# Kernel optimization log

Hardware: AMD Instinct MI355X
Metric: run time of the kernel (lower is better)

## Reference

```python
import jax, jax.numpy as jnp
import numpy as np

B = 32                 # decode batch (sequences)
NBLK = 128             # blocks per sequence
BLOCK = 16             # tokens per block
H, D = 16, 128         # heads, head_dim
HID = H * D            # 2048
FFN = 8192
VOCAB = 32000
MAXPOS = 8192
KV_LEN = NBLK * BLOCK  # 2048 max context
NUM_BLOCKS = B * NBLK  # 4096
ROPE_THETA = 10000.0


def _rope_cos_sin(pos):
    # pos: [...] int -> cos, sin: [..., D//2]
    inv_freq = 1.0 / (ROPE_THETA ** (jnp.arange(0, D, 2, dtype=jnp.float32) / D))
    ang = pos.astype(jnp.float32)[..., None] * inv_freq
    return jnp.cos(ang), jnp.sin(ang)


def _apply_rope(x, cos, sin):
    # x: [..., D]; cos/sin broadcastable to [..., D//2]; half-split (Llama) rotation
    x1, x2 = jnp.split(x, 2, axis=-1)
    return jnp.concatenate([x1 * cos - x2 * sin, x1 * sin + x2 * cos], axis=-1)


def setup_inputs() -> dict:
    key = jax.random.key(0)
    ks = jax.random.split(key, 12)
    inp = {
        "input_ids": jax.random.randint(ks[0], (B,), 0, VOCAB),
        "positions": jax.random.randint(ks[1], (B,), 0, KV_LEN),
        "kv_cache": jax.random.normal(ks[2], (NUM_BLOCKS, 2, BLOCK, H, D), jnp.float32),
        "block_tables": jnp.arange(NUM_BLOCKS, dtype=jnp.int32).reshape(B, NBLK),
        "context_lens": jax.random.randint(ks[3], (B,), 1, KV_LEN + 1).astype(jnp.int32),
        "embed_tokens": jax.random.normal(ks[4], (VOCAB, HID), jnp.float32) * 0.02,
        "embed_positions": jax.random.normal(ks[5], (MAXPOS, HID), jnp.float32) * 0.02,
        "Wq": jax.random.normal(ks[6], (HID, HID), jnp.float32) / np.float32(np.sqrt(HID)),
        "Wo": jax.random.normal(ks[7], (HID, HID), jnp.float32) / np.float32(np.sqrt(HID)),
        "Wprm": jax.random.normal(ks[8], (HID, HID), jnp.float32) / np.float32(np.sqrt(HID)),
        "W1": jax.random.normal(ks[9], (HID, FFN), jnp.float32) / np.float32(np.sqrt(HID)),
        "W2": jax.random.normal(ks[10], (FFN, HID), jnp.float32) / np.float32(np.sqrt(FFN)),
    }
    return inp


def reference(input_ids, positions, kv_cache, block_tables, context_lens,
              embed_tokens, embed_positions, Wq, Wo, Wprm, W1, W2):
    # token + position embeddings -> [B, HID]
    emb = embed_tokens[input_ids] + embed_positions[positions]

    # query projection with RoPE at the current position (fused RoPE on q)
    q = (emb @ Wq).reshape(B, H, D)
    cos_q, sin_q = _rope_cos_sin(positions)            # [B, D/2]
    q = _apply_rope(q, cos_q[:, None, :], sin_q[:, None, :])

    # paged KV gather: [B, NBLK, 2, BLOCK, H, D]
    kv = kv_cache[block_tables]
    k = kv[:, :, 0].reshape(B, KV_LEN, H, D)
    v = kv[:, :, 1].reshape(B, KV_LEN, H, D)

    # inline RoPE on gathered keys at their cache positions
    tok_pos = jnp.arange(KV_LEN)
    cos_k, sin_k = _rope_cos_sin(tok_pos)              # [S, D/2]
    k = _apply_rope(k, cos_k[None, :, None, :], sin_k[None, :, None, :])

    # decode attention over valid context
    scale = jnp.asarray(D, jnp.float32) ** -0.5
    scores = jnp.einsum("bhd,bshd->bhs", q, k) * scale
    valid = tok_pos[None, :] < context_lens[:, None]   # [B, S]
    scores = jnp.where(valid[:, None, :], scores, jnp.float32(-1e30))
    probs = jax.nn.softmax(scores, axis=-1)
    attn = jnp.einsum("bhs,bshd->bhd", probs, v).reshape(B, HID) @ Wo

    # PRM head + FFN (no activation in source), residual combine
    prm_scores = attn @ Wprm
    ffn_output = (attn @ W1) @ W2
    return ffn_output + prm_scores
```

## Files before the change

kernel.cpp:

```cpp
#include <hip/hip_runtime.h>
#include <hip/hip_bf16.h>
#include <math.h>

#define BATCH   32
#define NBLK    128
#define BLOCK_T 16
#define HEADS   16
#define DHEAD   128
#define HID     2048
#define FFN     8192
#define KV_LEN  2048

#define NSPLIT2 64
#define TOKSPL  32

__global__ void prep_kernel(const int* __restrict__ ids, const int* __restrict__ pos,
                            const float* __restrict__ et, const float* __restrict__ ep,
                            float* __restrict__ c4f, float* __restrict__ s4f,
                            float* __restrict__ emb) {
    if (blockIdx.x < 512) {
        int s = blockIdx.x * 4 + (threadIdx.x >> 6);
        int i = threadIdx.x & 63;
        float inv = powf(10000.0f, -(float)i / 64.0f);
        float ang = (float)s * inv;
        c4f[s * 64 + i] = cosf(ang);
        s4f[s * 64 + i] = sinf(ang);
    } else {
        int b = blockIdx.x - 512;
        int id = ids[b], p = pos[b];
        const float4* a = (const float4*)(et + (size_t)id * HID);
        const float4* d = (const float4*)(ep + (size_t)p * HID);
        float4* o = (float4*)(emb + (size_t)b * HID);
        for (int c = threadIdx.x; c < HID / 4; c += 256) {
            float4 x = a[c], y = d[c];
            o[c] = make_float4(x.x + y.x, x.y + y.y, x.z + y.z, x.w + y.w);
        }
    }
}

template <int KC>
__device__ __forceinline__ void gemm2_body(
    const float* __restrict__ X, const float* __restrict__ W,
    float* __restrict__ P, int K, int N, int bx, int by, int tid) {
    __shared__ float xs[KC][36];
    const int k0 = by * KC;
    const int j  = bx * 512 + tid * 2;

    #pragma unroll
    for (int t = tid; t < 32 * KC / 4; t += 256) {
        int bb = t / (KC / 4), qq = t % (KC / 4);
        float4 xv = *reinterpret_cast<const float4*>(X + (size_t)bb * K + k0 + 4 * qq);
        xs[4 * qq + 0][bb] = xv.x; xs[4 * qq + 1][bb] = xv.y;
        xs[4 * qq + 2][bb] = xv.z; xs[4 * qq + 3][bb] = xv.w;
    }
    __syncthreads();

    float acc[32][2];
    #pragma unroll
    for (int bb = 0; bb < 32; ++bb) { acc[bb][0] = 0.f; acc[bb][1] = 0.f; }

    const float* wp = W + (size_t)k0 * N + j;
    float2 bufA[16], bufB[16];
    #pragma unroll
    for (int u = 0; u < 16; ++u)
        bufA[u] = *reinterpret_cast<const float2*>(wp + (size_t)u * N);

    #define G2_FMA16(BUF, KK)                                                   \
        _Pragma("unroll")                                                       \
        for (int u = 0; u < 16; ++u) {                                          \
            const float2 w = BUF[u];                                            \
            _Pragma("unroll")                                                   \
            for (int g = 0; g < 8; ++g) {                                       \
                const float4 xv = *reinterpret_cast<const float4*>(&xs[(KK) + u][g * 4]); \
                acc[4*g+0][0] = fmaf(xv.x, w.x, acc[4*g+0][0]);                 \
                acc[4*g+0][1] = fmaf(xv.x, w.y, acc[4*g+0][1]);                 \
                acc[4*g+1][0] = fmaf(xv.y, w.x, acc[4*g+1][0]);                 \
                acc[4*g+1][1] = fmaf(xv.y, w.y, acc[4*g+1][1]);                 \
                acc[4*g+2][0] = fmaf(xv.z, w.x, acc[4*g+2][0]);                 \
                acc[4*g+2][1] = fmaf(xv.z, w.y, acc[4*g+2][1]);                 \
                acc[4*g+3][0] = fmaf(xv.w, w.x, acc[4*g+3][0]);                 \
                acc[4*g+3][1] = fmaf(xv.w, w.y, acc[4*g+3][1]);                 \
            }                                                                   \
        }

    for (int kk = 0; kk < KC; kk += 32) {
        #pragma unroll
        for (int u = 0; u < 16; ++u)
            bufB[u] = *reinterpret_cast<const float2*>(wp + (size_t)(kk + 16 + u) * N);
        G2_FMA16(bufA, kk)
        #pragma unroll
        for (int u = 0; u < 16; ++u) {
            int rr = kk + 32 + u; rr = (rr < KC) ? rr : (KC - 1);
            bufA[u] = *reinterpret_cast<const float2*>(wp + (size_t)rr * N);
        }
        G2_FMA16(bufB, kk + 16)
    }
    #undef G2_FMA16

    float* pp = P + ((size_t)by * 32) * N + j;
    #pragma unroll
    for (int bb = 0; bb < 32; ++bb)
        *reinterpret_cast<float2*>(pp + (size_t)bb * N) = make_float2(acc[bb][0], acc[bb][1]);
}

template <int KC>
__global__ __launch_bounds__(256) void gemm2_kernel(
    const float* __restrict__ X, const float* __restrict__ W,
    float* __restrict__ P, int K, int N) {
    gemm2_body<KC>(X, W, P, K, N, blockIdx.x, blockIdx.y, threadIdx.x);
}

__global__ __launch_bounds__(256) void gemm2_dual_kernel(
    const float* __restrict__ X, const float* __restrict__ Wprm,
    const float* __restrict__ W1,
    float* __restrict__ Pprm, float* __restrict__ P1) {
    if (blockIdx.x < 256) {
        gemm2_body<32>(X, Wprm, Pprm, HID, HID, blockIdx.x & 3, blockIdx.x >> 2, threadIdx.x);
    } else {
        int bb = blockIdx.x - 256;
        gemm2_body<128>(X, W1, P1, HID, FFN, bb & 15, bb >> 4, threadIdx.x);
    }
}

__global__ void red_stage1(const float* __restrict__ PA, const float* __restrict__ PB,
                           int ngA, float* __restrict__ S, int total4) {
    int idx4 = blockIdx.x * 256 + threadIdx.x;
    if (idx4 >= total4) return;
    int g = blockIdx.y;
    const float4* src = (const float4*)((g < ngA) ? PA : PB);
    int c0 = ((g < ngA) ? g : (g - ngA)) * 8;
    float4 s = make_float4(0.f, 0.f, 0.f, 0.f);
    #pragma unroll
    for (int c = 0; c < 8; ++c) {
        float4 v = src[(size_t)(c0 + c) * total4 + idx4];
        s.x += v.x; s.y += v.y; s.z += v.z; s.w += v.w;
    }
    ((float4*)S)[(size_t)g * total4 + idx4] = s;
}

__global__ void red_stage2(const float* __restrict__ S, int ng, int total4,
                           float* __restrict__ out) {
    int idx4 = blockIdx.x * 256 + threadIdx.x;
    if (idx4 >= total4) return;
    float4 s = make_float4(0.f, 0.f, 0.f, 0.f);
    for (int g = 0; g < ng; ++g) {
        float4 v = ((const float4*)S)[(size_t)g * total4 + idx4];
        s.x += v.x; s.y += v.y; s.z += v.z; s.w += v.w;
    }
    ((float4*)out)[idx4] = s;
}

__global__ void reduce4_kernel(const float* __restrict__ P, int nch, int total4,
                               float* __restrict__ out) {
    int idx4 = blockIdx.x * 256 + threadIdx.x;
    if (idx4 >= total4) return;
    const float4* P4 = (const float4*)P;
    float4 s = make_float4(0.f, 0.f, 0.f, 0.f);
    for (int c = 0; c < nch; ++c) {
        float4 v = P4[(size_t)c * total4 + idx4];
        s.x += v.x; s.y += v.y; s.z += v.z; s.w += v.w;
    }
    ((float4*)out)[idx4] = s;
}

__global__ void rope_q_from_S(const float* __restrict__ S, int ng,
                              const int* __restrict__ positions,
                              const float* __restrict__ c4f, const float* __restrict__ s4f,
                              float* __restrict__ qout) {
    int idx = blockIdx.x * 256 + threadIdx.x;
    int i = idx & 63, hh = (idx >> 6) & 15, b = idx >> 10;
    int base = b * HID + hh * DHEAD;
    float q1 = 0.f, q2 = 0.f;
    for (int g = 0; g < ng; ++g) {
        q1 += S[(size_t)g * (BATCH * HID) + base + i];
        q2 += S[(size_t)g * (BATCH * HID) + base + 64 + i];
    }
    int pos = positions[b];
    float co = c4f[pos * 64 + i], si = s4f[pos * 64 + i];
    qout[base + i]      = q1 * co - q2 * si;
    qout[base + 64 + i] = q1 * si + q2 * co;
}

__global__ __launch_bounds__(512) void attn_partial_kernel(
    const float* __restrict__ q, const float* __restrict__ kv,
    const int* __restrict__ block_tables, const int* __restrict__ context_lens,
    const float* __restrict__ c4f, const float* __restrict__ s4f,
    float* __restrict__ pm, float* __restrict__ pl, float* __restrict__ pacc) {
    const int idx = blockIdx.x;
    const int split = idx & (NSPLIT2 - 1);
    const int b = idx >> 6;
    const int tid = threadIdx.x;
    const int h = tid >> 5;
    const int l5 = tid & 31;

    const int ctx = context_lens[b];
    const int s_begin = split * TOKSPL;
    const int len = min(TOKSPL, ctx - s_begin);

    const int bt0 = block_tables[b * NBLK + split * 2];
    const int bt1 = block_tables[b * NBLK + split * 2 + 1];

    const int out_idx = (b * HEADS + h) * NSPLIT2 + split;

    const float4 qr = *reinterpret_cast<const float4*>(q + b * HID + h * DHEAD + 4 * l5);
    const float sgn2 = (l5 & 16) ? -1.f : 1.f;
    const int fq4 = (l5 & 15) * 4;
    float4 pqs;
    pqs.x = sgn2 * __shfl_xor(qr.x, 16); pqs.y = sgn2 * __shfl_xor(qr.y, 16);
    pqs.z = sgn2 * __shfl_xor(qr.z, 16); pqs.w = sgn2 * __shfl_xor(qr.w, 16);

    float m = -INFINITY, l = 0.f;
    float4 a4 = make_float4(0.f, 0.f, 0.f, 0.f);

    if (len > 0) {
        const int NI = (len + 3) & ~3;

        #define LOADT(T, K4, V4, C4, S4) {                                         \
            int tc = min((T), len - 1);                                            \
            int blk = (tc & 16) ? bt1 : bt0;                                       \
            const float* kp = kv + (size_t)blk * 65536                             \
                                 + (size_t)(tc & 15) * 2048 + h * DHEAD;           \
            K4 = *reinterpret_cast<const float4*>(kp + 4 * l5);                    \
            V4 = *reinterpret_cast<const float4*>(kp + 32768 + 4 * l5);            \
            C4 = *reinterpret_cast<const float4*>(c4f + (size_t)(s_begin + tc) * 64 + fq4); \
            S4 = *reinterpret_cast<const float4*>(s4f + (size_t)(s_begin + tc) * 64 + fq4); \
        }

        #define PROCT(T, K4, V4, C4, S4) {                                         \
            float cfx = fmaf(pqs.x, S4.x, qr.x * C4.x);                            \
            float cfy = fmaf(pqs.y, S4.y, qr.y * C4.y);                            \
            float cfz = fmaf(pqs.z, S4.z, qr.z * C4.z);                            \
            float cfw = fmaf(pqs.w, S4.w, qr.w * C4.w);                            \
            float dot = fmaf(K4.x, cfx, fmaf(K4.y, cfy, fmaf(K4.z, cfz, K4.w * cfw))); \
            dot += __shfl_xor(dot, 1);  dot += __shfl_xor(dot, 2);                 \
            dot += __shfl_xor(dot, 4);  dot += __shfl_xor(dot, 8);                 \
            dot += __shfl_xor(dot, 16);                                            \
            float d = ((T) < len) ? dot * 0.08838834764831845f : -INFINITY;        \
            float mn = fmaxf(m, d);                                                \
            float ms = fmaxf(mn, -3.0e38f);                                        \
            float corr = __expf(m - ms);                                           \
            float e = __expf(d - ms);                                              \
            l = l * corr + e;                                                      \
            a4.x = fmaf(e, V4.x, a4.x * corr);                                     \
            a4.y = fmaf(e, V4.y, a4.y * corr);                                     \
            a4.z = fmaf(e, V4.z, a4.z * corr);                                     \
            a4.w = fmaf(e, V4.w, a4.w * corr);                                     \
            m = mn;                                                                \
        }

        float4 kA, vA, cA, sA, kB, vB, cB, sB;
        float4 kC, vC, cC, sC, kD, vD, cD, sD;
        LOADT(0, kA, vA, cA, sA);
        LOADT(1, kB, vB, cB, sB);
        LOADT(2, kC, vC, cC, sC);
        LOADT(3, kD, vD, cD, sD);

        for (int t = 0; t < NI; t += 4) {
            PROCT(t,     kA, vA, cA, sA);  LOADT(t + 4, kA, vA, cA, sA);
            PROCT(t + 1, kB, vB, cB, sB);  LOADT(t + 5, kB, vB, cB, sB);
            PROCT(t + 2, kC, vC, cC, sC);  LOADT(t + 6, kC, vC, cC, sC);
            PROCT(t + 3, kD, vD, cD, sD);  LOADT(t + 7, kD, vD, cD, sD);
        }
        #undef LOADT
        #undef PROCT
    }

    if (l5 == 0) { pm[out_idx] = m; pl[out_idx] = l; }
    *reinterpret_cast<float4*>(pacc + (size_t)out_idx * 128 + 4 * l5) = a4;
}

__global__ void attn_combine_kernel(const float* __restrict__ pm, const float* __restrict__ pl,
                                    const float* __restrict__ pacc, float* __restrict__ attn_out) {
    const int bh = blockIdx.x;
    const int l5 = threadIdx.x;
    if (l5 >= 32) return;
    const int base = bh * NSPLIT2;
    float M = -INFINITY;
    for (int sp = 0; sp < NSPLIT2; ++sp) M = fmaxf(M, pm[base + sp]);
    float L = 0.f;
    float4 o = make_float4(0.f, 0.f, 0.f, 0.f);
    for (int sp = 0; sp < NSPLIT2; ++sp) {
        float mv = pm[base + sp];
        float ew = (mv == -INFINITY) ? 0.f : __expf(mv - M);
        L += pl[base + sp] * ew;
        float4 v = *reinterpret_cast<const float4*>(pacc + (size_t)(base + sp) * 128 + 4 * l5);
        o.x = fmaf(v.x, ew, o.x); o.y = fmaf(v.y, ew, o.y);
        o.z = fmaf(v.z, ew, o.z); o.w = fmaf(v.w, ew, o.w);
    }
    float inv = 1.f / L;
    *reinterpret_cast<float4*>(attn_out + bh * 128 + 4 * l5) =
        make_float4(o.x * inv, o.y * inv, o.z * inv, o.w * inv);
}

extern "C" void kernel_launch(void* const* d_in, const int* in_sizes, int n_in,
                              void* d_out, int out_size, void* d_ws, size_t ws_size,
                              hipStream_t stream) {
    const int*   input_ids    = (const int*)d_in[0];
    const int*   positions    = (const int*)d_in[1];
    const float* kv_cache     = (const float*)d_in[2];
    const int*   block_tables = (const int*)d_in[3];
    const int*   context_lens = (const int*)d_in[4];
    const float* embed_tokens = (const float*)d_in[5];
    const float* embed_pos    = (const float*)d_in[6];
    const float* Wq  = (const float*)d_in[7];
    const float* Wo  = (const float*)d_in[8];
    const float* Wprm= (const float*)d_in[9];
    const float* W1  = (const float*)d_in[10];
    const float* W2  = (const float*)d_in[11];
    float* out = (float*)d_out;

    char* ws = (char*)d_ws;
    size_t off = 0;
    float* c4f  = (float*)(ws + off); off += (size_t)KV_LEN * 64 * 4;
    float* s4f  = (float*)(ws + off); off += (size_t)KV_LEN * 64 * 4;
    float* emb  = (float*)(ws + off); off += (size_t)BATCH * HID * 4;
    float* qbuf = (float*)(ws + off); off += (size_t)BATCH * HID * 4;
    float* attn = (float*)(ws + off); off += (size_t)BATCH * HID * 4;
    float* ao   = (float*)(ws + off); off += (size_t)BATCH * HID * 4;
    float* h1   = (float*)(ws + off); off += (size_t)BATCH * FFN * 4;
    float* pm   = (float*)(ws + off); off += (size_t)BATCH * HEADS * NSPLIT2 * 4;
    float* plv  = (float*)(ws + off); off += (size_t)BATCH * HEADS * NSPLIT2 * 4;
    float* pacc = (float*)(ws + off); off += (size_t)BATCH * HEADS * NSPLIT2 * 128 * 4;
    float* S    = (float*)(ws + off); off += (size_t)16 * BATCH * HID * 4;
    float* P    = (float*)(ws + off); off += (size_t)64 * BATCH * FFN * 4;
    float* Pprm = (float*)(ws + off); off += (size_t)64 * BATCH * HID * 4;
    (void)ws_size; (void)in_sizes; (void)n_in; (void)out_size;

    const int T4_HID = BATCH * HID / 4;
    const int T4_FFN = BATCH * FFN / 4;

    prep_kernel<<<544, 256, 0, stream>>>(input_ids, positions, embed_tokens, embed_pos,
                                         c4f, s4f, emb);
    gemm2_kernel<32><<<dim3(4, 64), 256, 0, stream>>>(emb, Wq, P, HID, HID);
    red_stage1<<<dim3(64, 8), 256, 0, stream>>>(P, P, 8, S, T4_HID);
    rope_q_from_S<<<128, 256, 0, stream>>>(S, 8, positions, c4f, s4f, qbuf);
    attn_partial_kernel<<<BATCH * NSPLIT2, 512, 0, stream>>>(
        qbuf, kv_cache, block_tables, context_lens, c4f, s4f, pm, plv, pacc);
    attn_combine_kernel<<<BATCH * HEADS, 64, 0, stream>>>(pm, plv, pacc, attn);
    gemm2_kernel<32><<<dim3(4, 64), 256, 0, stream>>>(attn, Wo, P, HID, HID);
    red_stage1<<<dim3(64, 8), 256, 0, stream>>>(P, P, 8, S, T4_HID);
    red_stage2<<<64, 256, 0, stream>>>(S, 8, T4_HID, ao);
    gemm2_dual_kernel<<<512, 256, 0, stream>>>(ao, Wprm, W1, Pprm, P);
    reduce4_kernel<<<256, 256, 0, stream>>>(P, 16, T4_FFN, h1);
    gemm2_kernel<128><<<dim3(4, 64), 256, 0, stream>>>(h1, W2, P, FFN, HID);
    red_stage1<<<dim3(64, 16), 256, 0, stream>>>(P, Pprm, 8, S, T4_HID);
    red_stage2<<<64, 256, 0, stream>>>(S, 16, T4_HID, out);
}
```

Before: 285.4 us.

## Halve attention splits and replace two-stage split-K reductions with single-pass kernels

The attention split count drops from 64 to 32, so each block covers 64 tokens across four cache blocks, which halves the partial-result traffic for the combine step. The two-stage split-K reductions (red_stage1 + red_stage2) are replaced by single kernels that sum all 64 partial slices directly. The RoPE-q kernel now reads the GEMM partials itself, which removes several launches and the intermediate S buffer. The trade-off is fewer attention blocks (1024 instead of 2048) and single-pass reductions launched with only 64 threads per block, which may lower parallelism and memory-level concurrency.

```diff
diff --git a/kernel.cpp b/kernel.cpp
--- a/kernel.cpp
+++ b/kernel.cpp
@@ -11,8 +11,8 @@
 #define FFN     8192
 #define KV_LEN  2048
 
-#define NSPLIT2 64
-#define TOKSPL  32
+#define NSPLIT2 32
+#define TOKSPL  64
 
 __global__ void prep_kernel(const int* __restrict__ ids, const int* __restrict__ pos,
                             const float* __restrict__ et, const float* __restrict__ ep,
@@ -122,32 +122,40 @@
     }
 }
 
-__global__ void red_stage1(const float* __restrict__ PA, const float* __restrict__ PB,
-                           int ngA, float* __restrict__ S, int total4) {
-    int idx4 = blockIdx.x * 256 + threadIdx.x;
+__global__ void reduce64_kernel(const float* __restrict__ P, int total4,
+                                float* __restrict__ out) {
+    int idx4 = blockIdx.x * 64 + threadIdx.x;
     if (idx4 >= total4) return;
-    int g = blockIdx.y;
-    const float4* src = (const float4*)((g < ngA) ? PA : PB);
-    int c0 = ((g < ngA) ? g : (g - ngA)) * 8;
-    float4 s = make_float4(0.f, 0.f, 0.f, 0.f);
-    #pragma unroll
-    for (int c = 0; c < 8; ++c) {
-        float4 v = src[(size_t)(c0 + c) * total4 + idx4];
-        s.x += v.x; s.y += v.y; s.z += v.z; s.w += v.w;
-    }
-    ((float4*)S)[(size_t)g * total4 + idx4] = s;
-}
-
-__global__ void red_stage2(const float* __restrict__ S, int ng, int total4,
-                           float* __restrict__ out) {
-    int idx4 = blockIdx.x * 256 + threadIdx.x;
+    const float4* P4 = (const float4*)P;
+    float4 s0 = make_float4(0.f, 0.f, 0.f, 0.f);
+    float4 s1 = make_float4(0.f, 0.f, 0.f, 0.f);
+    #pragma unroll 8
+    for (int c = 0; c < 64; c += 2) {
+        float4 a = P4[(size_t)c * total4 + idx4];
+        float4 bv = P4[(size_t)(c + 1) * total4 + idx4];
+        s0.x += a.x; s0.y += a.y; s0.z += a.z; s0.w += a.w;
+        s1.x += bv.x; s1.y += bv.y; s1.z += bv.z; s1.w += bv.w;
+    }
+    ((float4*)out)[idx4] = make_float4(s0.x + s1.x, s0.y + s1.y, s0.z + s1.z, s0.w + s1.w);
+}
+
+__global__ void reduce_dual64_kernel(const float* __restrict__ PA,
+                                     const float* __restrict__ PB,
+                                     int total4, float* __restrict__ out) {
+    int idx4 = blockIdx.x * 64 + threadIdx.x;
     if (idx4 >= total4) return;
-    float4 s = make_float4(0.f, 0.f, 0.f, 0.f);
-    for (int g = 0; g < ng; ++g) {
-        float4 v = ((const float4*)S)[(size_t)g * total4 + idx4];
-        s.x += v.x; s.y += v.y; s.z += v.z; s.w += v.w;
-    }
-    ((float4*)out)[idx4] = s;
+    const float4* A = (const float4*)PA;
+    const float4* B = (const float4*)PB;
+    float4 s0 = make_float4(0.f, 0.f, 0.f, 0.f);
+    float4 s1 = make_float4(0.f, 0.f, 0.f, 0.f);
+    #pragma unroll 8
+    for (int c = 0; c < 64; ++c) {
+        float4 a = A[(size_t)c * total4 + idx4];
+        float4 bv = B[(size_t)c * total4 + idx4];
+        s0.x += a.x; s0.y += a.y; s0.z += a.z; s0.w += a.w;
+        s1.x += bv.x; s1.y += bv.y; s1.z += bv.z; s1.w += bv.w;
+    }
+    ((float4*)out)[idx4] = make_float4(s0.x + s1.x, s0.y + s1.y, s0.z + s1.z, s0.w + s1.w);
 }
 
 __global__ void reduce4_kernel(const float* __restrict__ P, int nch, int total4,
@@ -163,17 +171,18 @@
     ((float4*)out)[idx4] = s;
 }
 
-__global__ void rope_q_from_S(const float* __restrict__ S, int ng,
+__global__ void rope_q_from_P(const float* __restrict__ P,
                               const int* __restrict__ positions,
                               const float* __restrict__ c4f, const float* __restrict__ s4f,
                               float* __restrict__ qout) {
-    int idx = blockIdx.x * 256 + threadIdx.x;
+    int idx = blockIdx.x * 128 + threadIdx.x;
     int i = idx & 63, hh = (idx >> 6) & 15, b = idx >> 10;
     int base = b * HID + hh * DHEAD;
     float q1 = 0.f, q2 = 0.f;
-    for (int g = 0; g < ng; ++g) {
-        q1 += S[(size_t)g * (BATCH * HID) + base + i];
-        q2 += S[(size_t)g * (BATCH * HID) + base + 64 + i];
+    #pragma unroll 8
+    for (int c = 0; c < 64; ++c) {
+        q1 += P[(size_t)c * (BATCH * HID) + base + i];
+        q2 += P[(size_t)c * (BATCH * HID) + base + 64 + i];
     }
     int pos = positions[b];
     float co = c4f[pos * 64 + i], si = s4f[pos * 64 + i];
@@ -188,7 +197,7 @@
     float* __restrict__ pm, float* __restrict__ pl, float* __restrict__ pacc) {
     const int idx = blockIdx.x;
     const int split = idx & (NSPLIT2 - 1);
-    const int b = idx >> 6;
+    const int b = idx >> 5;
     const int tid = threadIdx.x;
     const int h = tid >> 5;
     const int l5 = tid & 31;
@@ -197,8 +206,10 @@
     const int s_begin = split * TOKSPL;
     const int len = min(TOKSPL, ctx - s_begin);
 
-    const int bt0 = block_tables[b * NBLK + split * 2];
-    const int bt1 = block_tables[b * NBLK + split * 2 + 1];
+    const int bt0 = block_tables[b * NBLK + split * 4];
+    const int bt1 = block_tables[b * NBLK + split * 4 + 1];
+    const int bt2 = block_tables[b * NBLK + split * 4 + 2];
+    const int bt3 = block_tables[b * NBLK + split * 4 + 3];
 
     const int out_idx = (b * HEADS + h) * NSPLIT2 + split;
 
@@ -217,7 +228,9 @@
 
         #define LOADT(T, K4, V4, C4, S4) {                                         \
             int tc = min((T), len - 1);                                            \
-            int blk = (tc & 16) ? bt1 : bt0;                                       \
+            int blkLo = (tc & 16) ? bt1 : bt0;                                     \
+            int blkHi = (tc & 16) ? bt3 : bt2;                                     \
+            int blk = (tc & 32) ? blkHi : blkLo;                                   \
             const float* kp = kv + (size_t)blk * 65536                             \
                                  + (size_t)(tc & 15) * 2048 + h * DHEAD;           \
             K4 = *reinterpret_cast<const float4*>(kp + 4 * l5);                    \
@@ -321,8 +334,8 @@
     float* pm   = (float*)(ws + off); off += (size_t)BATCH * HEADS * NSPLIT2 * 4;
     float* plv  = (float*)(ws + off); off += (size_t)BATCH * HEADS * NSPLIT2 * 4;
     float* pacc = (float*)(ws + off); off += (size_t)BATCH * HEADS * NSPLIT2 * 128 * 4;
-    float* S    = (float*)(ws + off); off += (size_t)16 * BATCH * HID * 4;
-    float* P    = (float*)(ws + off); off += (size_t)64 * BATCH * FFN * 4;
+    float* P    = (float*)(ws + off); off += (size_t)64 * BATCH * HID * 4;
+    float* P1   = (float*)(ws + off); off += (size_t)16 * BATCH * FFN * 4;
     float* Pprm = (float*)(ws + off); off += (size_t)64 * BATCH * HID * 4;
     (void)ws_size; (void)in_sizes; (void)n_in; (void)out_size;
 
@@ -332,17 +345,14 @@
     prep_kernel<<<544, 256, 0, stream>>>(input_ids, positions, embed_tokens, embed_pos,
                                          c4f, s4f, emb);
     gemm2_kernel<32><<<dim3(4, 64), 256, 0, stream>>>(emb, Wq, P, HID, HID);
-    red_stage1<<<dim3(64, 8), 256, 0, stream>>>(P, P, 8, S, T4_HID);
-    rope_q_from_S<<<128, 256, 0, stream>>>(S, 8, positions, c4f, s4f, qbuf);
+    rope_q_from_P<<<256, 128, 0, stream>>>(P, positions, c4f, s4f, qbuf);
     attn_partial_kernel<<<BATCH * NSPLIT2, 512, 0, stream>>>(
         qbuf, kv_cache, block_tables, context_lens, c4f, s4f, pm, plv, pacc);
     attn_combine_kernel<<<BATCH * HEADS, 64, 0, stream>>>(pm, plv, pacc, attn);
     gemm2_kernel<32><<<dim3(4, 64), 256, 0, stream>>>(attn, Wo, P, HID, HID);
-    red_stage1<<<dim3(64, 8), 256, 0, stream>>>(P, P, 8, S, T4_HID);
-    red_stage2<<<64, 256, 0, stream>>>(S, 8, T4_HID, ao);
-    gemm2_dual_kernel<<<512, 256, 0, stream>>>(ao, Wprm, W1, Pprm, P);
-    reduce4_kernel<<<256, 256, 0, stream>>>(P, 16, T4_FFN, h1);
+    reduce64_kernel<<<256, 64, 0, stream>>>(P, T4_HID, ao);
+    gemm2_dual_kernel<<<512, 256, 0, stream>>>(ao, Wprm, W1, Pprm, P1);
+    reduce4_kernel<<<256, 256, 0, stream>>>(P1, 16, T4_FFN, h1);
     gemm2_kernel<128><<<dim3(4, 64), 256, 0, stream>>>(h1, W2, P, FFN, HID);
-    red_stage1<<<dim3(64, 16), 256, 0, stream>>>(P, Pprm, 8, S, T4_HID);
-    red_stage2<<<64, 256, 0, stream>>>(S, 16, T4_HID, out);
-}
+    reduce_dual64_kernel<<<256, 64, 0, stream>>>(P, Pprm, T4_HID, out);
+}
```

After: 308.1 us. 1.08x slower.
